# Kernel tuning notes

Measured on AMD Instinct MI355X. Metric: run time of the kernel, lower is better.

The kernel has to match this reference:

```python
import jax, jax.numpy as jnp
import numpy as np

N_NODES = 100000
N_EDGES = 1600000
C_IN = 500
HIDDEN = 256
C_OUT = 50
K = 10
K_HALF = K // 2  # 5
ALPHA = 0.1


def _prop(x, src, dst, norm, n):
    # one propagate(): gather source features, scale by edge norm, scatter-add to dst
    msg = norm[:, None] * x[src]          # [E, F]
    return jax.ops.segment_sum(msg, dst, num_segments=n)


def setup_inputs() -> dict:
    key = jax.random.key(0)
    k0, k1, k2, k3 = jax.random.split(key, 4)
    x = jax.random.normal(k0, (N_NODES, C_IN), dtype=jnp.float32)
    edge_index = jax.random.randint(k1, (2, N_EDGES), 0, N_NODES, dtype=jnp.int32)
    # temp[k] = alpha * (1-alpha)^(2k), k = 0..K//2  (even-order PPR coefficients)
    temp = jnp.asarray(ALPHA * (1.0 - ALPHA) ** (2 * np.arange(K_HALF + 1)), dtype=jnp.float32)
    W1 = jax.random.normal(k2, (C_IN, HIDDEN), dtype=jnp.float32) / np.sqrt(C_IN).astype(np.float32)
    b1 = jnp.zeros((HIDDEN,), jnp.float32)
    W2 = jax.random.normal(k3, (HIDDEN, C_OUT), dtype=jnp.float32) / np.sqrt(HIDDEN).astype(np.float32)
    b2 = jnp.zeros((C_OUT,), jnp.float32)
    return {"x": x, "edge_index": edge_index, "W1": W1, "b1": b1, "W2": W2, "b2": b2, "temp": temp}


def reference(x, edge_index, W1, b1, W2, b2, temp):
    n = x.shape[0]
    src, dst = edge_index[0], edge_index[1]
    # sym-normalized adjacency A_hat = D^-1/2 A D^-1/2.
    # (get_laplacian 'sym' then add_self_loops(-norm, 1.0): the -1/+1 diagonal
    #  entries cancel under scatter-add, leaving exactly A_hat.)
    deg = jax.ops.segment_sum(jnp.ones_like(src, dtype=x.dtype), src, num_segments=n)
    dinv = jnp.where(deg > 0, jax.lax.rsqrt(jnp.maximum(deg, 1e-12)), 0.0)
    norm = dinv[src] * dinv[dst]          # [E]

    # MLP (dropout is identity in eval mode)
    h = jax.nn.relu(x @ W1 + b1)
    h = h @ W2 + b2                        # [N, C_OUT]

    hidden0 = h * temp[0]

    def body(k, carry):
        xk, hid = carry
        xk = _prop(xk, src, dst, norm, n)  # A_hat @ x
        xk = _prop(xk, src, dst, norm, n)  # A_hat^2 @ x
        hid = hid + temp[k + 1] * xk
        return (xk, hid)

    _, hidden = jax.lax.fori_loop(0, K_HALF, body, (h, hidden0))
    return jax.nn.log_softmax(hidden, axis=1)
```

## Files before the change

kernel.cpp:

```cpp
#include <hip/hip_runtime.h>

#define NN 100000
#define CIN 500
#define KPAD 512
#define HID 256
#define COUT 50
#define NPADOUT 64
#define FPAD 64

#define NBLK 256
#define CB 128
#define NC ((NN + CB - 1) / CB)
#define NCB (NC * NBLK)
#define NCB2 (2 * NCB)

typedef __attribute__((ext_vector_type(8))) short short8;
typedef __attribute__((ext_vector_type(4))) float f32x4;

static __device__ __forceinline__ unsigned short f2bf(float f) {
  union { float f; unsigned u; } v; v.f = f;
  unsigned r = (v.u + 0x7fffu + ((v.u >> 16) & 1u)) >> 16;
  return (unsigned short)r;
}

static __device__ __forceinline__ int slotAt(const int* __restrict__ incl,
                                             const int* __restrict__ bpre, int g) {
  return g ? incl[g - 1] + bpre[(g - 1) >> 10] : 0;
}


__launch_bounds__(256)
__global__ void k_p1(const int* __restrict__ src, const int* __restrict__ dst,
                     int* __restrict__ blk_cnt, int E, int chunk) {
  __shared__ int bd[NC], bs[NC];
  int tid = threadIdx.x;
  for (int i = tid; i < NC; i += 256) { bd[i] = 0; bs[i] = 0; }
  __syncthreads();
  int e0 = blockIdx.x * chunk, e1 = min(E, e0 + chunk);
  for (int e = e0 + tid; e < e1; e += 256) {
    atomicAdd(&bd[dst[e] >> 7], 1);
    atomicAdd(&bs[src[e] >> 7], 1);
  }
  __syncthreads();
  for (int i = tid; i < NC; i += 256) {
    blk_cnt[i * NBLK + blockIdx.x] = bd[i];
    blk_cnt[NCB + i * NBLK + blockIdx.x] = bs[i];
  }
}


__global__ void k_scan_a(const int* __restrict__ hist, int* __restrict__ incl,
                         int* __restrict__ bsum, int n) {
  __shared__ int ts[256];
  int tid = threadIdx.x;
  int base = blockIdx.x * 1024 + tid * 4;
  int a0 = 0, a1 = 0, a2 = 0, a3 = 0;
  if (base + 3 < n) {
    a0 = hist[base]; a1 = hist[base + 1]; a2 = hist[base + 2]; a3 = hist[base + 3];
  } else {
    if (base     < n) a0 = hist[base];
    if (base + 1 < n) a1 = hist[base + 1];
    if (base + 2 < n) a2 = hist[base + 2];
    if (base + 3 < n) a3 = hist[base + 3];
  }
  a1 += a0; a2 += a1; a3 += a2;
  ts[tid] = a3;
  __syncthreads();
  for (int o = 1; o < 256; o <<= 1) {
    int v = ts[tid];
    if (tid >= o) v += ts[tid - o];
    __syncthreads();
    ts[tid] = v;
    __syncthreads();
  }
  int ex = tid ? ts[tid - 1] : 0;
  if (base     < n) incl[base]     = a0 + ex;
  if (base + 1 < n) incl[base + 1] = a1 + ex;
  if (base + 2 < n) incl[base + 2] = a2 + ex;
  if (base + 3 < n) incl[base + 3] = a3 + ex;
  if (tid == 255) bsum[blockIdx.x] = ts[255];
}

__global__ void k_scan_b(const int* __restrict__ bsum, int* __restrict__ bpre, int nb) {
  __shared__ int s[512];
  int tid = threadIdx.x;
  s[tid] = (tid < nb) ? bsum[tid] : 0;
  __syncthreads();
  for (int o = 1; o < 512; o <<= 1) {
    int v = s[tid];
    if (tid >= o) v += s[tid - o];
    __syncthreads();
    s[tid] = v;
    __syncthreads();
  }
  if (tid < nb) bpre[tid] = tid ? s[tid - 1] : 0;
}


__launch_bounds__(256)
__global__ void k_p2(const int* __restrict__ src, const int* __restrict__ dst,
                     const int* __restrict__ incl, const int* __restrict__ bpre,
                     int* __restrict__ pkd, unsigned char* __restrict__ pks, int E, int chunk) {
  __shared__ int cd[NC], cs[NC];
  int tid = threadIdx.x;
  for (int i = tid; i < NC; i += 256) {
    cd[i] = slotAt(incl, bpre, i * NBLK + blockIdx.x);
    cs[i] = slotAt(incl, bpre, NCB + i * NBLK + blockIdx.x) - E;
  }
  __syncthreads();
  int e0 = blockIdx.x * chunk, e1 = min(E, e0 + chunk);
  for (int e = e0 + tid; e < e1; e += 256) {
    int s = src[e], d = dst[e];
    int pd = atomicAdd(&cd[d >> 7], 1);
    pkd[pd] = (s << 7) | (d & 127);
    int ps = atomicAdd(&cs[s >> 7], 1);
    pks[ps] = (unsigned char)(s & 127);
  }
}


__launch_bounds__(256)
__global__ void k_p3s(const int* __restrict__ incl, const int* __restrict__ bpre,
                      const unsigned char* __restrict__ pks, float* __restrict__ dinv, int E) {
  __shared__ int hist[CB];
  int b = blockIdx.x, tid = threadIdx.x;
  if (tid < CB) hist[tid] = 0;
  __syncthreads();
  int s0 = slotAt(incl, bpre, NCB + b * NBLK) - E;
  int s1 = slotAt(incl, bpre, NCB + (b + 1) * NBLK) - E;
  for (int e = s0 + tid; e < s1; e += 256) atomicAdd(&hist[pks[e]], 1);
  __syncthreads();
  if (tid < CB) {
    int node = b * CB + tid;
    if (node < NN) {
      int c = hist[tid];
      dinv[node] = c > 0 ? rsqrtf((float)c) : 0.f;
    }
  }
}


__launch_bounds__(256)
__global__ void k_p3d(const int* __restrict__ incl, const int* __restrict__ bpre,
                      const int* __restrict__ pkd, const float* __restrict__ dinv,
                      int* __restrict__ offs, int2* __restrict__ epk, int E) {
  __shared__ int hist[CB], base[CB], cur[CB];
  int b = blockIdx.x, tid = threadIdx.x;
  if (tid < CB) hist[tid] = 0;
  __syncthreads();
  int s0 = slotAt(incl, bpre, b * NBLK);
  int s1 = slotAt(incl, bpre, (b + 1) * NBLK);
  for (int e = s0 + tid; e < s1; e += 256) atomicAdd(&hist[pkd[e] & 127], 1);
  __syncthreads();
  if (tid == 0) {
    int acc = s0;
    for (int i = 0; i < CB; i++) { base[i] = acc; cur[i] = acc; acc += hist[i]; }
  }
  __syncthreads();
  if (tid < CB) {
    int node = b * CB + tid;
    if (node < NN) offs[node] = base[tid];
  }
  if (b == gridDim.x - 1 && tid == 0) offs[NN] = E;
  for (int e = s0 + tid; e < s1; e += 256) {
    int pk = pkd[e];
    int fine = pk & 127, s = pk >> 7;
    int pos = atomicAdd(&cur[fine], 1);
    float nm = dinv[s] * dinv[b * CB + fine];
    epk[pos] = make_int2(s, __float_as_int(nm));
  }
}


__global__ void k_wt(const float* __restrict__ W1, const float* __restrict__ W2,
                     unsigned short* __restrict__ W1T, unsigned short* __restrict__ W2T) {
  int idx = blockIdx.x * 256 + threadIdx.x;
  if (idx < HID * KPAD) {
    int n = idx >> 9, k = idx & 511;
    W1T[idx] = (k < CIN) ? f2bf(W1[(long)k * HID + n]) : (unsigned short)0;
  } else if (idx < HID * KPAD + NPADOUT * HID) {
    int i2 = idx - HID * KPAD;
    int n = i2 >> 8, k = i2 & 255;
    W2T[i2] = (n < COUT) ? f2bf(W2[(long)k * COUT + n]) : (unsigned short)0;
  }
}


__launch_bounds__(512)
__global__ void k_mlp(const float* __restrict__ X, const unsigned short* __restrict__ W1T,
                      const float* __restrict__ b1, const unsigned short* __restrict__ W2T,
                      const float* __restrict__ b2, const float* __restrict__ temp,
                      unsigned short* __restrict__ X0B, float* __restrict__ HIDB) {
  __shared__ unsigned short smem[64 * 264];
  unsigned short* As = smem;
  unsigned short* Bs = smem + 128 * 40;
  const int tid = threadIdx.x;
  const int lane = tid & 63, w = tid >> 6;
  const int wr = w >> 2, wc = w & 3;
  const int row0 = blockIdx.x * 128;
  f32x4 acc[4][4] = {};
  const int sr = tid >> 3, sc = tid & 7;
  const int br = tid >> 2, bc = tid & 3;

  for (int kk = 0; kk < KPAD; kk += 32) {
    __syncthreads();
#pragma unroll
    for (int p = 0; p < 2; p++) {
      int r = sr + p * 64;
      int grow = row0 + r;
      int gk = kk + sc * 4;
      ushort4 val;
      if (grow < NN && gk < CIN) {
        const float4 f = *reinterpret_cast<const float4*>(&X[(long)grow * CIN + gk]);
        val.x = f2bf(f.x); val.y = f2bf(f.y); val.z = f2bf(f.z); val.w = f2bf(f.w);
      } else {
        val.x = val.y = val.z = val.w = 0;
      }
      *reinterpret_cast<ushort4*>(&As[r * 40 + sc * 4]) = val;
    }
#pragma unroll
    for (int p = 0; p < 2; p++) {
      int nl = br + p * 128;
      const uint4 v = *reinterpret_cast<const uint4*>(&W1T[(long)nl * KPAD + kk + bc * 8]);
      *reinterpret_cast<uint4*>(&Bs[nl * 40 + bc * 8]) = v;
    }
    __syncthreads();
    short8 af[4], bfr[4];
    const int koff = (lane >> 4) * 8;
#pragma unroll
    for (int i = 0; i < 4; i++)
      af[i] = *reinterpret_cast<const short8*>(&As[(wr * 64 + i * 16 + (lane & 15)) * 40 + koff]);
#pragma unroll
    for (int j = 0; j < 4; j++)
      bfr[j] = *reinterpret_cast<const short8*>(&Bs[(wc * 64 + j * 16 + (lane & 15)) * 40 + koff]);
#pragma unroll
    for (int i = 0; i < 4; i++)
#pragma unroll
      for (int j = 0; j < 4; j++)
        acc[i][j] = __builtin_amdgcn_mfma_f32_16x16x32_bf16(af[i], bfr[j], acc[i][j], 0, 0, 0);
  }

  unsigned short* Hs = smem;
  const float t0 = temp[0];
  const int rt = w >> 1;
  const int jh = w & 1;
#pragma unroll
  for (int ph = 0; ph < 2; ph++) {
    __syncthreads();
    if (wr == ph) {
#pragma unroll
      for (int i = 0; i < 4; i++) {
        int lr = i * 16 + (lane >> 4) * 4;
#pragma unroll
        for (int j = 0; j < 4; j++) {
          int col = wc * 64 + j * 16 + (lane & 15);
          float bv = b1[col];
#pragma unroll
          for (int r = 0; r < 4; r++) {
            float v = acc[i][j][r] + bv;
            v = v > 0.f ? v : 0.f;
            Hs[(lr + r) * 264 + col] = f2bf(v);
          }
        }
      }
    }
    __syncthreads();
    f32x4 acc2[2] = {};
    const int koff = (lane >> 4) * 8;
    for (int kk = 0; kk < HID; kk += 32) {
      short8 a = *reinterpret_cast<const short8*>(&Hs[(rt * 16 + (lane & 15)) * 264 + kk + koff]);
#pragma unroll
      for (int jj = 0; jj < 2; jj++) {
        int n = (jh * 2 + jj) * 16 + (lane & 15);
        short8 b = *reinterpret_cast<const short8*>(&W2T[n * HID + kk + koff]);
        acc2[jj] = __builtin_amdgcn_mfma_f32_16x16x32_bf16(a, b, acc2[jj], 0, 0, 0);
      }
    }
#pragma unroll
    for (int jj = 0; jj < 2; jj++) {
      int col = (jh * 2 + jj) * 16 + (lane & 15);
      float bv = (col < COUT) ? b2[col] : 0.f;
#pragma unroll
      for (int r = 0; r < 4; r++) {
        int row = row0 + ph * 64 + rt * 16 + (lane >> 4) * 4 + r;
        if (row < NN) {
          float v = acc2[jj][r] + bv;
          X0B[((long)row << 6) + col] = f2bf(v);
          if (col < COUT) HIDB[(long)row * COUT + col] = t0 * v;
        }
      }
    }
  }
}


__launch_bounds__(256)
__global__ void k_prop(const int* __restrict__ offs, const int2* __restrict__ epk,
                       const unsigned short* __restrict__ xin,
                       unsigned short* __restrict__ xout, float* __restrict__ hid,
                       const float* __restrict__ temp, int accidx) {
  int node = blockIdx.x * 8 + (threadIdx.x >> 5);
  if (node >= NN) return;
  int h = threadIdx.x & 31;
  int fp = h * 2;
  int s0 = offs[node], s1 = offs[node + 1];
  float a0 = 0.f, a1 = 0.f;
  int e = s0;
  for (; e + 7 < s1; e += 8) {
    int2 p[8];
#pragma unroll
    for (int q = 0; q < 8; q++) p[q] = epk[e + q];
    unsigned v[8];
#pragma unroll
    for (int q = 0; q < 8; q++)
      v[q] = *reinterpret_cast<const unsigned*>(&xin[((long)p[q].x << 6) + fp]);
#pragma unroll
    for (int q = 0; q < 8; q++) {
      float wq = __int_as_float(p[q].y);
      a0 += wq * __uint_as_float(v[q] << 16);
      a1 += wq * __uint_as_float(v[q] & 0xffff0000u);
    }
  }
  for (; e + 3 < s1; e += 4) {
    int2 p0 = epk[e], p1 = epk[e + 1], p2 = epk[e + 2], p3 = epk[e + 3];
    unsigned v0 = *reinterpret_cast<const unsigned*>(&xin[((long)p0.x << 6) + fp]);
    unsigned v1 = *reinterpret_cast<const unsigned*>(&xin[((long)p1.x << 6) + fp]);
    unsigned v2 = *reinterpret_cast<const unsigned*>(&xin[((long)p2.x << 6) + fp]);
    unsigned v3 = *reinterpret_cast<const unsigned*>(&xin[((long)p3.x << 6) + fp]);
    float w0 = __int_as_float(p0.y), w1 = __int_as_float(p1.y);
    float w2 = __int_as_float(p2.y), w3 = __int_as_float(p3.y);
    a0 += w0 * __uint_as_float(v0 << 16) + w1 * __uint_as_float(v1 << 16)
        + w2 * __uint_as_float(v2 << 16) + w3 * __uint_as_float(v3 << 16);
    a1 += w0 * __uint_as_float(v0 & 0xffff0000u) + w1 * __uint_as_float(v1 & 0xffff0000u)
        + w2 * __uint_as_float(v2 & 0xffff0000u) + w3 * __uint_as_float(v3 & 0xffff0000u);
  }
  for (; e < s1; e++) {
    int2 p0 = epk[e];
    float w0 = __int_as_float(p0.y);
    unsigned v0 = *reinterpret_cast<const unsigned*>(&xin[((long)p0.x << 6) + fp]);
    a0 += w0 * __uint_as_float(v0 << 16);
    a1 += w0 * __uint_as_float(v0 & 0xffff0000u);
  }
  if (fp < COUT) {
    unsigned pk = ((unsigned)f2bf(a1) << 16) | (unsigned)f2bf(a0);
    *reinterpret_cast<unsigned*>(&xout[((long)node << 6) + fp]) = pk;
    if (accidx >= 0) {
      float t = temp[accidx];
      float2* hp = reinterpret_cast<float2*>(&hid[(long)node * COUT + fp]);
      float2 o = *hp;
      o.x += t * a0; o.y += t * a1;
      *hp = o;
    }
  }
}


__launch_bounds__(256)
__global__ void k_lsm(const float* __restrict__ hid, float* __restrict__ out) {
  int node = blockIdx.x * 4 + (threadIdx.x >> 6);
  if (node >= NN) return;
  int f = threadIdx.x & 63;
  float v = (f < COUT) ? hid[(long)node * COUT + f] : -INFINITY;
  float m = v;
#pragma unroll
  for (int o = 32; o > 0; o >>= 1) m = fmaxf(m, __shfl_xor(m, o, 64));
  float ex = (f < COUT) ? expf(v - m) : 0.f;
  float s = ex;
#pragma unroll
  for (int o = 32; o > 0; o >>= 1) s += __shfl_xor(s, o, 64);
  if (f < COUT) out[(long)node * COUT + f] = (v - m) - logf(s);
}


extern "C" void kernel_launch(void* const* d_in, const int* in_sizes, int n_in,
                              void* d_out, int out_size, void* d_ws, size_t ws_size,
                              hipStream_t stream) {
  const float* X  = (const float*)d_in[0];
  const int* EI   = (const int*)d_in[1];
  const float* W1 = (const float*)d_in[2];
  const float* B1 = (const float*)d_in[3];
  const float* W2 = (const float*)d_in[4];
  const float* B2 = (const float*)d_in[5];
  const float* TEMP = (const float*)d_in[6];
  const int E = in_sizes[1] / 2;
  const int* src = EI;
  const int* dst = EI + E;

  char* ws = (char*)d_ws;
  size_t off = 0;
  auto alloc = [&](size_t bytes) -> void* {
    off = (off + 511) & ~(size_t)511;
    void* p = ws + off;
    off += bytes;
    return p;
  };
  unsigned short* W1T = (unsigned short*)alloc((size_t)HID * KPAD * 2);
  unsigned short* W2T = (unsigned short*)alloc((size_t)NPADOUT * HID * 2);
  unsigned short* X0B = (unsigned short*)alloc((size_t)NN * FPAD * 2);
  unsigned short* X1B = (unsigned short*)alloc((size_t)NN * FPAD * 2);
  float* HIDB = (float*)alloc((size_t)NN * COUT * 4);
  float* DINV = (float*)alloc((size_t)NN * 4);
  int* OFFS   = (int*)alloc((size_t)(NN + 1) * 4);
  int* BLKC   = (int*)alloc((size_t)NCB2 * 4);
  int* INCL   = (int*)alloc((size_t)NCB2 * 4);
  int* BSUM   = (int*)alloc(512 * 4);
  int* BPRE   = (int*)alloc(512 * 4);
  int* PKD    = (int*)alloc((size_t)E * 4);
  unsigned char* PKS = (unsigned char*)alloc((size_t)E);
  int2* EPK   = (int2*)alloc((size_t)E * 8);

  const int chunk = (E + NBLK - 1) / NBLK;
  const int nsa = (NCB2 + 1023) / 1024;

  k_p1<<<NBLK, 256, 0, stream>>>(src, dst, BLKC, E, chunk);
  k_scan_a<<<nsa, 256, 0, stream>>>(BLKC, INCL, BSUM, NCB2);
  k_scan_b<<<1, 512, 0, stream>>>(BSUM, BPRE, nsa);
  k_p2<<<NBLK, 256, 0, stream>>>(src, dst, INCL, BPRE, PKD, PKS, E, chunk);
  k_p3s<<<NC, 256, 0, stream>>>(INCL, BPRE, PKS, DINV, E);
  k_p3d<<<NC, 256, 0, stream>>>(INCL, BPRE, PKD, DINV, OFFS, EPK, E);

  k_wt<<<(HID * KPAD + NPADOUT * HID + 255) / 256, 256, 0, stream>>>(W1, W2, W1T, W2T);

  k_mlp<<<(NN + 127) / 128, 512, 0, stream>>>(X, W1T, B1, W2T, B2, TEMP, X0B, HIDB);

  const int PB = (NN + 7) / 8;
  for (int k = 0; k < 5; k++) {
    k_prop<<<PB, 256, 0, stream>>>(OFFS, EPK, X0B, X1B, HIDB, TEMP, -1);
    k_prop<<<PB, 256, 0, stream>>>(OFFS, EPK, X1B, X0B, HIDB, TEMP, k + 1);
  }
  k_lsm<<<(NN + 3) / 4, 256, 0, stream>>>(HIDB, (float*)d_out);
}
```

Measured before the change: 907.9 us.

## Double-buffer LDS tiles and prefetch next K-slice into registers in MLP GEMM

The first-layer GEMM in the MLP kernel now stages global loads for the next 32-wide K slice into registers while the MFMAs for the current slice run. It alternates between two LDS buffers, so only one barrier is needed per iteration instead of two. This is meant to hide global memory latency behind compute. In exchange it uses more LDS and registers per block, which may reduce occupancy.

```diff
diff --git a/kernel.cpp b/kernel.cpp
--- a/kernel.cpp
+++ b/kernel.cpp
@@ -191,9 +191,7 @@
                       const float* __restrict__ b1, const unsigned short* __restrict__ W2T,
                       const float* __restrict__ b2, const float* __restrict__ temp,
                       unsigned short* __restrict__ X0B, float* __restrict__ HIDB) {
-  __shared__ unsigned short smem[64 * 264];
-  unsigned short* As = smem;
-  unsigned short* Bs = smem + 128 * 40;
+  __shared__ unsigned short smem[2 * 15360];
   const int tid = threadIdx.x;
   const int lane = tid & 63, w = tid >> 6;
   const int wr = w >> 2, wc = w & 3;
@@ -202,29 +200,46 @@
   const int sr = tid >> 3, sc = tid & 7;
   const int br = tid >> 2, bc = tid & 3;
 
-  for (int kk = 0; kk < KPAD; kk += 32) {
-    __syncthreads();
-#pragma unroll
-    for (int p = 0; p < 2; p++) {
-      int r = sr + p * 64;
-      int grow = row0 + r;
+  float4 ra0, ra1;
+  uint4 rb0, rb1;
+
+  auto load_regs = [&](int kk) {
+    {
+      int grow = row0 + sr;
       int gk = kk + sc * 4;
-      ushort4 val;
-      if (grow < NN && gk < CIN) {
-        const float4 f = *reinterpret_cast<const float4*>(&X[(long)grow * CIN + gk]);
-        val.x = f2bf(f.x); val.y = f2bf(f.y); val.z = f2bf(f.z); val.w = f2bf(f.w);
-      } else {
-        val.x = val.y = val.z = val.w = 0;
-      }
-      *reinterpret_cast<ushort4*>(&As[r * 40 + sc * 4]) = val;
-    }
-#pragma unroll
-    for (int p = 0; p < 2; p++) {
-      int nl = br + p * 128;
-      const uint4 v = *reinterpret_cast<const uint4*>(&W1T[(long)nl * KPAD + kk + bc * 8]);
-      *reinterpret_cast<uint4*>(&Bs[nl * 40 + bc * 8]) = v;
-    }
-    __syncthreads();
+      if (grow < NN && gk < CIN)
+        ra0 = *reinterpret_cast<const float4*>(&X[(long)grow * CIN + gk]);
+      else { ra0.x = ra0.y = ra0.z = ra0.w = 0.f; }
+    }
+    {
+      int grow = row0 + sr + 64;
+      int gk = kk + sc * 4;
+      if (grow < NN && gk < CIN)
+        ra1 = *reinterpret_cast<const float4*>(&X[(long)grow * CIN + gk]);
+      else { ra1.x = ra1.y = ra1.z = ra1.w = 0.f; }
+    }
+    rb0 = *reinterpret_cast<const uint4*>(&W1T[(long)br * KPAD + kk + bc * 8]);
+    rb1 = *reinterpret_cast<const uint4*>(&W1T[(long)(br + 128) * KPAD + kk + bc * 8]);
+  };
+
+  auto write_lds = [&](unsigned short* As, unsigned short* Bs) {
+    ushort4 v0, v1;
+    v0.x = f2bf(ra0.x); v0.y = f2bf(ra0.y); v0.z = f2bf(ra0.z); v0.w = f2bf(ra0.w);
+    v1.x = f2bf(ra1.x); v1.y = f2bf(ra1.y); v1.z = f2bf(ra1.z); v1.w = f2bf(ra1.w);
+    *reinterpret_cast<ushort4*>(&As[sr * 40 + sc * 4]) = v0;
+    *reinterpret_cast<ushort4*>(&As[(sr + 64) * 40 + sc * 4]) = v1;
+    *reinterpret_cast<uint4*>(&Bs[br * 40 + bc * 8]) = rb0;
+    *reinterpret_cast<uint4*>(&Bs[(br + 128) * 40 + bc * 8]) = rb1;
+  };
+
+  load_regs(0);
+#pragma unroll 2
+  for (int t = 0; t < 16; t++) {
+    unsigned short* As = smem + (t & 1) * 15360;
+    unsigned short* Bs = As + 128 * 40;
+    write_lds(As, Bs);
+    __syncthreads();
+    if (t < 15) load_regs((t + 1) * 32);
     short8 af[4], bfr[4];
     const int koff = (lane >> 4) * 8;
 #pragma unroll
```

New measurement: 876.1 us. 1.04x faster.

## Double-buffer LDS and register-prefetch X/W1 tiles in MLP GEMM

Applied to the files above, without the earlier changes.

The first-layer GEMM k-loop now uses two LDS buffers and two sets of prefetch registers. Global loads for tile k+2 are issued before computing tile k, which removes one barrier per iteration and overlaps memory latency with MFMA work. This uses more registers and LDS, which may reduce occupancy. Only the MLP kernel changes, while the propagation kernels, which probably dominate the runtime, are untouched.

```diff
diff --git a/kernel.cpp b/kernel.cpp
--- a/kernel.cpp
+++ b/kernel.cpp
@@ -186,14 +186,52 @@
 }
 
 
+#define LOADS(ra0_, ra1_, rb0_, rb1_, kkc)                                        \
+  {                                                                               \
+    const int kk_ = (kkc);                                                        \
+    bool okk = kk_ + sc * 4 <= 496;                                               \
+    if (okA && okk) ra0_ = *reinterpret_cast<const float4*>(&X[xbaseA + kk_]);    \
+    else { ra0_.x = ra0_.y = ra0_.z = ra0_.w = 0.f; }                             \
+    if (okB && okk) ra1_ = *reinterpret_cast<const float4*>(&X[xbaseB + kk_]);    \
+    else { ra1_.x = ra1_.y = ra1_.z = ra1_.w = 0.f; }                             \
+    rb0_ = *reinterpret_cast<const uint4*>(&W1T[wbase0 + kk_]);                   \
+    rb1_ = *reinterpret_cast<const uint4*>(&W1T[wbase1 + kk_]);                   \
+  }
+
+#define STORE_LDS(As_, Bs_, ra0_, ra1_, rb0_, rb1_)                               \
+  {                                                                               \
+    ushort4 v0, v1;                                                               \
+    v0.x = f2bf(ra0_.x); v0.y = f2bf(ra0_.y); v0.z = f2bf(ra0_.z); v0.w = f2bf(ra0_.w); \
+    v1.x = f2bf(ra1_.x); v1.y = f2bf(ra1_.y); v1.z = f2bf(ra1_.z); v1.w = f2bf(ra1_.w); \
+    *reinterpret_cast<ushort4*>(&As_[sr * 40 + sc * 4]) = v0;                     \
+    *reinterpret_cast<ushort4*>(&As_[(sr + 64) * 40 + sc * 4]) = v1;              \
+    *reinterpret_cast<uint4*>(&Bs_[br * 40 + bc * 8]) = rb0_;                     \
+    *reinterpret_cast<uint4*>(&Bs_[(br + 128) * 40 + bc * 8]) = rb1_;             \
+  }
+
+#define COMPUTE(As_, Bs_)                                                         \
+  {                                                                               \
+    short8 af[4], bfr[4];                                                         \
+    const int koff = (lane >> 4) * 8;                                             \
+    _Pragma("unroll")                                                             \
+    for (int i = 0; i < 4; i++)                                                   \
+      af[i] = *reinterpret_cast<const short8*>(&As_[(wr * 64 + i * 16 + (lane & 15)) * 40 + koff]); \
+    _Pragma("unroll")                                                             \
+    for (int j = 0; j < 4; j++)                                                   \
+      bfr[j] = *reinterpret_cast<const short8*>(&Bs_[(wc * 64 + j * 16 + (lane & 15)) * 40 + koff]); \
+    _Pragma("unroll")                                                             \
+    for (int i = 0; i < 4; i++)                                                   \
+      _Pragma("unroll")                                                           \
+      for (int j = 0; j < 4; j++)                                                 \
+        acc[i][j] = __builtin_amdgcn_mfma_f32_16x16x32_bf16(af[i], bfr[j], acc[i][j], 0, 0, 0); \
+  }
+
 __launch_bounds__(512)
 __global__ void k_mlp(const float* __restrict__ X, const unsigned short* __restrict__ W1T,
                       const float* __restrict__ b1, const unsigned short* __restrict__ W2T,
                       const float* __restrict__ b2, const float* __restrict__ temp,
                       unsigned short* __restrict__ X0B, float* __restrict__ HIDB) {
-  __shared__ unsigned short smem[64 * 264];
-  unsigned short* As = smem;
-  unsigned short* Bs = smem + 128 * 40;
+  __shared__ unsigned short smem[2 * 15360];
   const int tid = threadIdx.x;
   const int lane = tid & 63, w = tid >> 6;
   const int wr = w >> 2, wc = w & 3;
@@ -202,42 +240,39 @@
   const int sr = tid >> 3, sc = tid & 7;
   const int br = tid >> 2, bc = tid & 3;
 
-  for (int kk = 0; kk < KPAD; kk += 32) {
-    __syncthreads();
-#pragma unroll
-    for (int p = 0; p < 2; p++) {
-      int r = sr + p * 64;
-      int grow = row0 + r;
-      int gk = kk + sc * 4;
-      ushort4 val;
-      if (grow < NN && gk < CIN) {
-        const float4 f = *reinterpret_cast<const float4*>(&X[(long)grow * CIN + gk]);
-        val.x = f2bf(f.x); val.y = f2bf(f.y); val.z = f2bf(f.z); val.w = f2bf(f.w);
-      } else {
-        val.x = val.y = val.z = val.w = 0;
-      }
-      *reinterpret_cast<ushort4*>(&As[r * 40 + sc * 4]) = val;
-    }
-#pragma unroll
-    for (int p = 0; p < 2; p++) {
-      int nl = br + p * 128;
-      const uint4 v = *reinterpret_cast<const uint4*>(&W1T[(long)nl * KPAD + kk + bc * 8]);
-      *reinterpret_cast<uint4*>(&Bs[nl * 40 + bc * 8]) = v;
-    }
-    __syncthreads();
-    short8 af[4], bfr[4];
-    const int koff = (lane >> 4) * 8;
-#pragma unroll
-    for (int i = 0; i < 4; i++)
-      af[i] = *reinterpret_cast<const short8*>(&As[(wr * 64 + i * 16 + (lane & 15)) * 40 + koff]);
-#pragma unroll
-    for (int j = 0; j < 4; j++)
-      bfr[j] = *reinterpret_cast<const short8*>(&Bs[(wc * 64 + j * 16 + (lane & 15)) * 40 + koff]);
-#pragma unroll
-    for (int i = 0; i < 4; i++)
-#pragma unroll
-      for (int j = 0; j < 4; j++)
-        acc[i][j] = __builtin_amdgcn_mfma_f32_16x16x32_bf16(af[i], bfr[j], acc[i][j], 0, 0, 0);
+  float4 raA0, raA1; uint4 rbA0, rbA1;
+  float4 raB0, raB1; uint4 rbB0, rbB1;
+
+  const int growA = row0 + sr;
+  const int growB = row0 + sr + 64;
+  const bool okA = growA < NN, okB = growB < NN;
+  const long xbaseA = (long)growA * CIN + sc * 4;
+  const long xbaseB = (long)growB * CIN + sc * 4;
+  const long wbase0 = (long)br * KPAD + bc * 8;
+  const long wbase1 = (long)(br + 128) * KPAD + bc * 8;
+
+  LOADS(raA0, raA1, rbA0, rbA1, 0);
+  LOADS(raB0, raB1, rbB0, rbB1, 32);
+
+#pragma unroll
+  for (int tt = 0; tt < 8; tt++) {
+    const int kk0 = tt * 64;
+    {
+      unsigned short* As = smem;
+      unsigned short* Bs = smem + 128 * 40;
+      STORE_LDS(As, Bs, raA0, raA1, rbA0, rbA1);
+      __syncthreads();
+      if (kk0 + 64 < KPAD) LOADS(raA0, raA1, rbA0, rbA1, kk0 + 64);
+      COMPUTE(As, Bs);
+    }
+    {
+      unsigned short* As = smem + 15360;
+      unsigned short* Bs = As + 128 * 40;
+      STORE_LDS(As, Bs, raB0, raB1, rbB0, rbB1);
+      __syncthreads();
+      if (kk0 + 96 < KPAD) LOADS(raB0, raB1, rbB0, rbB1, kk0 + 96);
+      COMPUTE(As, Bs);
+    }
   }
 
   unsigned short* Hs = smem;
```

After: 863.9 us. 1.05x faster.
